# Kernel optimization log

Hardware: AMD Instinct MI355X
Metric: run time of the kernel (lower is better)

Reference implementation:

```python
import jax, jax.numpy as jnp
import numpy as np
import math

B, S, D, H = 4, 1024, 1024, 16
HD = D // H  # 64
DFF = 4 * D
LN_EPS = 1e-5

def setup_inputs() -> dict:
    key = jax.random.key(0)
    ks = jax.random.split(key, 24)
    sd = lambda fi, fo: 1.0 / math.sqrt(fi)
    def lin(k, fi, fo):
        k1, k2 = jax.random.split(k)
        w = jax.random.uniform(k1, (fi, fo), jnp.float32, -sd(fi, fo), sd(fi, fo))
        b = jax.random.uniform(k2, (fo,), jnp.float32, -sd(fi, fo), sd(fi, fo))
        return w, b
    x = jax.random.normal(ks[0], (B, S, D), jnp.float32)
    Wk, bk = lin(ks[1], D, D)
    Wq, bq = lin(ks[2], D, D)
    Wv, bv = lin(ks[3], D, D)
    # per-head projections stacked over heads: [H, D, HD]
    def head_lin(k):
        kk = jax.random.split(k, H)
        ws, bs = zip(*[lin(kk[h], D, HD) for h in range(H)])
        return jnp.stack(ws), jnp.stack(bs)
    Whq, bhq = head_lin(ks[4])
    Whk, bhk = head_lin(ks[5])
    Whv, bhv = head_lin(ks[6])
    Wo, bo = lin(ks[7], D, D)
    W1, b1 = lin(ks[8], D, DFF)
    W2, b2 = lin(ks[9], DFF, D)
    gamma = jnp.ones((D,), jnp.float32)
    beta = jnp.zeros((D,), jnp.float32)
    return dict(x=x, Wk=Wk, bk=bk, Wq=Wq, bq=bq, Wv=Wv, bv=bv,
                Whq=Whq, bhq=bhq, Whk=Whk, bhk=bhk, Whv=Whv, bhv=bhv,
                Wo=Wo, bo=bo, W1=W1, b1=b1, W2=W2, b2=b2,
                gamma=gamma, beta=beta)

def _layer_norm(x, gamma, beta):
    mu = jnp.mean(x, axis=-1, keepdims=True)
    var = jnp.mean(jnp.square(x - mu), axis=-1, keepdims=True)
    return (x - mu) * jax.lax.rsqrt(var + LN_EPS) * gamma + beta

def reference(x, Wk, bk, Wq, bq, Wv, bv, Whq, bhq, Whk, bhk, Whv, bhv,
              Wo, bo, W1, b1, W2, b2, gamma, beta):
    # outer projections; NOTE: forward passes (k, q, v) into MHA, so the
    # MHA 'Q' stream is k_proj(x), 'K' stream is q_proj(x), 'V' is v_proj(x)
    ko = x @ Wk + bk
    qo = x @ Wq + bq
    vo = x @ Wv + bv
    # per-head projections (batched over heads): [B,H,S,HD]
    q = jnp.einsum('bsd,hde->bhse', ko, Whq) + bhq[None, :, None, :]
    k = jnp.einsum('bsd,hde->bhse', qo, Whk) + bhk[None, :, None, :]
    v = jnp.einsum('bsd,hde->bhse', vo, Whv) + bhv[None, :, None, :]
    # NOTE: original scales by sqrt(d_model), not sqrt(head_dim)
    scores = jnp.einsum('bhse,bhte->bhst', q, k) / math.sqrt(D)
    w = jax.nn.softmax(scores, axis=-1)
    o = jnp.einsum('bhst,bhte->bhse', w, v)         # [B,H,S,HD]
    o = o.transpose(0, 2, 1, 3).reshape(B, S, D)    # concat heads
    attn = o @ Wo + bo
    # dropout is identity in eval; shared LayerNorm after both residuals
    r1 = _layer_norm(x + attn, gamma, beta)
    ff = jax.nn.gelu(r1 @ W1 + b1, approximate=False) @ W2 + b2
    out = _layer_norm(r1 + ff, gamma, beta)
    return out
```

## Files before the change

kernel.cpp:

```cpp
#include <hip/hip_runtime.h>
#include <cstdint>
#include <cstddef>

#define D_MODEL 1024
#define SEQ 1024
#define BATCH 4
#define NHEAD 16
#define HDIM 64
#define ROWS (BATCH*SEQ)

typedef unsigned short u16;
typedef __attribute__((ext_vector_type(4))) unsigned short u16x4;
typedef __attribute__((ext_vector_type(8))) unsigned short u16x8;
typedef __attribute__((ext_vector_type(8))) __bf16 bf16x8v;
typedef __attribute__((ext_vector_type(4))) float f32x4;

__device__ inline u16 f2bf(float f){
  union{float f; unsigned u;} c; c.f = f;
  unsigned r = c.u + 0x7FFFu + ((c.u>>16)&1u);
  return (u16)(r>>16);
}
__device__ inline float bf2f(u16 s){
  union{unsigned u; float f;} c; c.u = ((unsigned)s)<<16; return c.f;
}
__device__ inline float gelu_f(float x){ return 0.5f*x*(1.f+erff(x*0.7071067811865475f)); }

__device__ __forceinline__ void gload_lds16(const void* g, void* l){
  __builtin_amdgcn_global_load_lds(
    (const __attribute__((address_space(1))) unsigned int*)g,
    (__attribute__((address_space(3))) unsigned int*)l, 16, 0, 0);
}

__global__ __launch_bounds__(256) void convert_bf(const float* __restrict__ in, u16* __restrict__ out){
  size_t idx = (size_t)blockIdx.x*256 + threadIdx.x;
  f32x4 v = *(const f32x4*)(in + idx*4);
  u16x4 o = { f2bf(v.x), f2bf(v.y), f2bf(v.z), f2bf(v.w) };
  *(u16x4*)(out + idx*4) = o;
}

__global__ __launch_bounds__(256) void transpose_conv(const float* __restrict__ W, u16* __restrict__ WT, int K, int N){
  __shared__ float tile[32][33];
  int n0 = blockIdx.x*32, k0 = blockIdx.y*32;
  int tx = threadIdx.x & 31, ty = threadIdx.x >> 5;
  #pragma unroll
  for (int i=0;i<4;i++){
    int r = ty + i*8;
    tile[r][tx] = W[(size_t)(k0+r)*N + n0 + tx];
  }
  __syncthreads();
  #pragma unroll
  for (int i=0;i<4;i++){
    int r = ty + i*8;
    WT[(size_t)(n0+r)*K + k0 + tx] = f2bf(tile[tx][r]);
  }
}

__global__ __launch_bounds__(256) void head_transpose(const float* __restrict__ Wh, u16* __restrict__ WT){
  __shared__ float tile[32][33];
  int d0 = blockIdx.x*32, e0 = blockIdx.y*32, h = blockIdx.z;
  int tx = threadIdx.x & 31, ty = threadIdx.x >> 5;
  #pragma unroll
  for (int i=0;i<4;i++){
    int r = ty + i*8;
    tile[r][tx] = Wh[(size_t)h*D_MODEL*HDIM + (size_t)(d0+r)*HDIM + e0 + tx];
  }
  __syncthreads();
  #pragma unroll
  for (int i=0;i<4;i++){
    int r = ty + i*8;
    WT[(size_t)(h*HDIM + e0 + r)*D_MODEL + d0 + tx] = f2bf(tile[tx][r]);
  }
}

__global__ __launch_bounds__(256) void bias_cat(const float* a, const float* b, const float* c, float* o){
  int i = blockIdx.x*256 + threadIdx.x;
  float v = (i < 1024) ? a[i] : (i < 2048) ? b[i-1024] : c[i-2048];
  o[i] = v;
}

__device__ __forceinline__ void phase16(const u16* Ah, const u16* Bh,
  f32x4 acc[8][4], int mq, int nq, int wr, int wc, int fr, int kg)
{
  bf16x8v af[2][4], bfv[2][2];
  #pragma unroll
  for (int ks=0;ks<2;ks++){
    #pragma unroll
    for (int mf=0;mf<4;mf++){
      int r = wr*64 + mf*16 + fr;
      af[ks][mf] = *(const bf16x8v*)&Ah[r*64 + (((kg+4*ks)^(r&7)))*8];
    }
    #pragma unroll
    for (int nf=0;nf<2;nf++){
      int r = wc*32 + nf*16 + fr;
      bfv[ks][nf] = *(const bf16x8v*)&Bh[r*64 + (((kg+4*ks)^(r&7)))*8];
    }
  }
  __builtin_amdgcn_s_setprio(1);
  #pragma unroll
  for (int ks=0;ks<2;ks++)
    #pragma unroll
    for (int mf=0;mf<4;mf++)
      #pragma unroll
      for (int nf=0;nf<2;nf++)
        acc[mq*4+mf][nq*2+nf] =
          __builtin_amdgcn_mfma_f32_16x16x32_bf16(af[ks][mf], bfv[ks][nf], acc[mq*4+mf][nq*2+nf], 0,0,0);
  __builtin_amdgcn_s_setprio(0);
}

__global__ __launch_bounds__(512,2) void gemm256_8p(
  const u16* __restrict__ A, const u16* __restrict__ BT, const float* __restrict__ bias,
  u16* __restrict__ outB, int N, int K, int mode, int act)
{
  __shared__ __align__(16) u16 As[2][2][128*64];
  __shared__ __align__(16) u16 Bs[2][2][128*64];
  int t = threadIdx.x, lane = t&63, wid = t>>6;
  int wr = wid>>2, wc = wid&3;
  int fr = lane&15, kg = lane>>4;
  int gx = gridDim.x;
  int bid = blockIdx.y*gx + blockIdx.x;
  int nwg = gx*gridDim.y;
  int cpx = nwg>>3;
  int sw = (bid&7)*cpx + (bid>>3);
  int tc = sw % gx, tr = sw / gx;

  const u16* Abase = A  + (size_t)tr*256*K;
  const u16* Bbase = BT + (size_t)tc*256*K;
  int srow = lane>>3, sch8 = lane&7;

  f32x4 acc[8][4];
  #pragma unroll
  for (int m=0;m<8;m++)
    #pragma unroll
    for (int n=0;n<4;n++) acc[m][n] = (f32x4)0.f;

  #define STAGE_A8(buf,h,kt) { _Pragma("unroll") for (int li=0;li<2;li++){ \
    int sr = (wid*2+li)*8 + srow; \
    int gr = ((sr>>6)<<7) + (h)*64 + (sr&63); \
    int sc = sch8 ^ (sr&7); \
    gload_lds16(Abase + (size_t)gr*K + (size_t)(kt)*64 + sc*8, &As[buf][h][(wid*2+li)*512]); } }
  #define STAGE_B8(buf,h,kt) { _Pragma("unroll") for (int li=0;li<2;li++){ \
    int sr = (wid*2+li)*8 + srow; \
    int gc = ((sr>>5)<<6) + (h)*32 + (sr&31); \
    int sc = sch8 ^ (sr&7); \
    gload_lds16(Bbase + (size_t)gc*K + (size_t)(kt)*64 + sc*8, &Bs[buf][h][(wid*2+li)*512]); } }
  #define BAR asm volatile("s_barrier" ::: "memory")

  int NT = K >> 6;
  STAGE_A8(0,0,0); STAGE_B8(0,0,0); STAGE_B8(0,1,0); STAGE_A8(0,1,0);
  asm volatile("s_waitcnt vmcnt(4)" ::: "memory");

  for (int kt=0; kt<NT; ++kt){
    int buf = kt&1, nb = buf^1;
    int pre = (kt+1 < NT);
    if (pre) STAGE_A8(nb,0,kt+1);
    BAR;
    phase16(&As[buf][0][0], &Bs[buf][0][0], acc, 0,0, wr,wc,fr,kg);
    BAR;
    if (pre){ STAGE_B8(nb,0,kt+1); asm volatile("s_waitcnt vmcnt(6)" ::: "memory"); }
    else    { asm volatile("s_waitcnt vmcnt(2)" ::: "memory"); }
    BAR;
    phase16(&As[buf][0][0], &Bs[buf][1][0], acc, 0,1, wr,wc,fr,kg);
    BAR;
    if (pre){ STAGE_B8(nb,1,kt+1); asm volatile("s_waitcnt vmcnt(6)" ::: "memory"); }
    else    { asm volatile("s_waitcnt vmcnt(0)" ::: "memory"); }
    BAR;
    phase16(&As[buf][1][0], &Bs[buf][0][0], acc, 1,0, wr,wc,fr,kg);
    BAR;
    if (pre){ STAGE_A8(nb,1,kt+1); asm volatile("s_waitcnt vmcnt(4)" ::: "memory"); }
    BAR;
    phase16(&As[buf][1][0], &Bs[buf][1][0], acc, 1,1, wr,wc,fr,kg);
    BAR;
  }

  int crow0 = tr*256 + wr*128;
  int ccol0 = tc*256 + wc*64;
  #pragma unroll
  for (int n=0;n<4;n++){
    int col = ccol0 + n*16 + fr;
    float bv = bias[mode==0 ? col : (col & (N-1))];
    #pragma unroll
    for (int m=0;m<8;m++){
      int rbase = crow0 + m*16 + kg*4;
      #pragma unroll
      for (int i=0;i<4;i++){
        float v = acc[m][n][i] + bv;
        if (act) v = gelu_f(v);
        int row = rbase + i;
        if (mode == 0)
          outB[(size_t)(col>>10)*((size_t)ROWS*1024) + (size_t)row*1024 + (col&1023)] = f2bf(v);
        else
          outB[(size_t)row*N + col] = f2bf(v);
      }
    }
  }
}

__device__ __forceinline__ void stage128(u16 (*As)[4096], u16 (*Bs)[4096], int b,
  const u16* Ab, const u16* Bb, int Kstride, int kt, int wid, int rr, int sch)
{
  #pragma unroll
  for (int c=0;c<2;c++){
    int reg = c*4 + wid;
    int row = reg*16 + rr;
    gload_lds16(Ab + (size_t)row*Kstride + kt*32 + sch*8, &As[b][reg*512]);
  }
  #pragma unroll
  for (int c=0;c<2;c++){
    int reg = c*4 + wid;
    int row = reg*16 + rr;
    gload_lds16(Bb + (size_t)row*Kstride + kt*32 + sch*8, &Bs[b][reg*512]);
  }
}

__device__ __forceinline__ void gemm128_core(u16 (*As)[4096], u16 (*Bs)[4096],
  const u16* __restrict__ A, const u16* __restrict__ BT, const float* __restrict__ bias,
  float* __restrict__ outF, u16* __restrict__ outB,
  int N, int Kstride, int kofs, int Ksub, int mode, int act, int addbias)
{
  int t = threadIdx.x, lane = t&63, wid = t>>6;
  int wr = wid>>1, wc = wid&1;
  int fr = lane&15, kg = lane>>4;
  int gx = gridDim.x;
  int bid = blockIdx.y*gx + blockIdx.x;
  int nwg = gx*gridDim.y;
  int cpx = nwg >> 3;
  int sw = (bid&7)*cpx + (bid>>3);
  int tc = sw % gx, tr = sw / gx;

  const u16* Ab = A  + (size_t)tr*128*Kstride + kofs;
  const u16* Bb = BT + (size_t)tc*128*Kstride + kofs;
  int rr = lane>>2, cc = lane&3;
  int sch = cc ^ ((rr>>1)&3);

  f32x4 acc[4][4];
  #pragma unroll
  for (int m=0;m<4;m++)
    #pragma unroll
    for (int n=0;n<4;n++) acc[m][n] = (f32x4)0.f;

  int NT = Ksub >> 5;

  stage128(As, Bs, 0, Ab, Bb, Kstride, 0, wid, rr, sch);
  stage128(As, Bs, 1, Ab, Bb, Kstride, 1, wid, rr, sch);
  int buf = 0;
  for (int kt=0; kt<NT; ++kt){
    if (kt+2 < NT){
      int nb = buf+2; if (nb>=3) nb-=3;
      stage128(As, Bs, nb, Ab, Bb, Kstride, kt+2, wid, rr, sch);
      asm volatile("s_waitcnt vmcnt(8)" ::: "memory");
    } else if (kt+1 < NT){
      asm volatile("s_waitcnt vmcnt(4)" ::: "memory");
    } else {
      asm volatile("s_waitcnt vmcnt(0)" ::: "memory");
    }
    asm volatile("s_barrier" ::: "memory");
    bf16x8v af[4], bfv[4];
    #pragma unroll
    for (int m=0;m<4;m++){
      int r = wr*64 + m*16 + fr;
      af[m] = *(const bf16x8v*)&As[buf][r*32 + (kg ^ ((r>>1)&3))*8];
    }
    #pragma unroll
    for (int n=0;n<4;n++){
      int r = wc*64 + n*16 + fr;
      bfv[n] = *(const bf16x8v*)&Bs[buf][r*32 + (kg ^ ((r>>1)&3))*8];
    }
    #pragma unroll
    for (int m=0;m<4;m++)
      #pragma unroll
      for (int n=0;n<4;n++)
        acc[m][n] = __builtin_amdgcn_mfma_f32_16x16x32_bf16(af[m], bfv[n], acc[m][n], 0,0,0);
    if (kt+1 < NT)
      asm volatile("s_barrier" ::: "memory");
    buf += 1; if (buf >= 3) buf = 0;
  }

  int crow0 = tr*128 + wr*64;
  int ccol0 = tc*128 + wc*64;
  #pragma unroll
  for (int n=0;n<4;n++){
    int col = ccol0 + n*16 + fr;
    float bv = addbias ? bias[col] : 0.f;
    #pragma unroll
    for (int m=0;m<4;m++){
      int rbase = crow0 + m*16 + kg*4;
      #pragma unroll
      for (int i=0;i<4;i++){
        float v = acc[m][n][i] + bv;
        if (act) v = gelu_f(v);
        int row = rbase + i;
        if (mode == 0){
          outB[(size_t)(col>>10)*((size_t)ROWS*1024) + (size_t)row*1024 + (col&1023)] = f2bf(v);
        } else if (mode == 1){
          outB[(size_t)row*N + col] = f2bf(v);
        } else if (mode == 2){
          int b = row >> 10, s = row & 1023;
          int h = col >> 6, e = col & 63;
          outB[(((size_t)((b*NHEAD + h)*HDIM + e))<<10) + s] = f2bf(v);
        } else {
          outF[(size_t)row*1024 + col] = v;
        }
      }
    }
  }
}

__global__ __launch_bounds__(256) void g_gemm_sk(
  const u16* A, const u16* BT, const float* bias, float* outBase, int K)
{
  __shared__ __align__(16) u16 As[3][4096];
  __shared__ __align__(16) u16 Bs[3][4096];
  int z = blockIdx.z;
  int Ksub = K >> 1;
  gemm128_core(As, Bs, A, BT, bias, outBase + (size_t)z*ROWS*1024, nullptr,
               1024, K, z*Ksub, Ksub, 3, 0, z==0);
}

struct B3 { const u16* A[3]; const u16* BT[3]; const float* bias[3]; u16* Cb[3]; int mode[3]; };
__global__ __launch_bounds__(256) void g_gemm_b3(B3 p){
  __shared__ __align__(16) u16 As[3][4096];
  __shared__ __align__(16) u16 Bs[3][4096];
  int z = blockIdx.z;
  gemm128_core(As, Bs, p.A[z], p.BT[z], p.bias[z], nullptr, p.Cb[z],
               1024, 1024, 0, 1024, p.mode[z], 0, 1);
}

__global__ __launch_bounds__(256) void attn_mfma(const u16* __restrict__ Q, const u16* __restrict__ Km,
                                                 const u16* __restrict__ Vt, u16* __restrict__ O)
{
  __shared__ __align__(16) u16 Ks[64*64];
  __shared__ __align__(16) u16 Vs[64*64];
  __shared__ __align__(16) u16 Ps[4][16*64];
  int t = threadIdx.x, lane = t & 63, wid = t >> 6;
  int fr = lane & 15, kg = lane >> 4;
  int qt = blockIdx.x, h = blockIdx.y, b = blockIdx.z;
  const size_t qkbase = ((size_t)b*SEQ)*D_MODEL + (size_t)h*HDIM;
  const size_t vtb = ((size_t)(b*NHEAD + h))*HDIM*SEQ;

  int qrow = qt*64 + wid*16 + fr;
  bf16x8v aq[2];
  aq[0] = *(const bf16x8v*)(Q + qkbase + (size_t)qrow*D_MODEL + kg*8);
  aq[1] = *(const bf16x8v*)(Q + qkbase + (size_t)qrow*D_MODEL + 32 + kg*8);

  f32x4 Oacc[4];
  #pragma unroll
  for (int n=0;n<4;n++) Oacc[n] = (f32x4)0.f;
  float m_run[4], l_run[4];
  #pragma unroll
  for (int i=0;i<4;i++){ m_run[i] = -3e38f; l_run[i] = 0.f; }

  int srow = lane >> 3;
  int sch  = (lane & 7) ^ srow;
  int x7 = fr & 7;

  for (int kt = 0; kt < SEQ/64; ++kt){
    #pragma unroll
    for (int c=0;c<2;c++){
      int r0 = (wid*2 + c)*8;
      int rowk = r0 + srow;
      gload_lds16(Km + qkbase + (size_t)(kt*64 + rowk)*D_MODEL + sch*8, &Ks[r0*64]);
      gload_lds16(Vt + vtb + (size_t)rowk*SEQ + kt*64 + sch*8, &Vs[r0*64]);
    }
    __syncthreads();

    f32x4 z4 = (f32x4)0.f;
    f32x4 s4[4];
    #pragma unroll
    for (int n=0;n<4;n++){
      int r = n*16 + fr;
      bf16x8v k0v = *(const bf16x8v*)&Ks[r*64 + ((kg  ) ^ x7)*8];
      bf16x8v k1v = *(const bf16x8v*)&Ks[r*64 + ((4+kg) ^ x7)*8];
      s4[n] = __builtin_amdgcn_mfma_f32_16x16x32_bf16(aq[0], k0v, z4, 0,0,0);
      s4[n] = __builtin_amdgcn_mfma_f32_16x16x32_bf16(aq[1], k1v, s4[n], 0,0,0);
      s4[n] *= 0.03125f;
    }

    float mI[4], sc[4], ls[4], p[4][4];
    #pragma unroll
    for (int i=0;i<4;i++)
      mI[i] = fmaxf(fmaxf(s4[0][i], s4[1][i]), fmaxf(s4[2][i], s4[3][i]));
    #pragma unroll
    for (int off=1; off<16; off<<=1){
      #pragma unroll
      for (int i=0;i<4;i++) mI[i] = fmaxf(mI[i], __shfl_xor(mI[i], off));
    }
    #pragma unroll
    for (int i=0;i<4;i++){
      float m_new = fmaxf(m_run[i], mI[i]);
      sc[i] = __expf(m_run[i] - m_new);
      m_run[i] = m_new;
      ls[i] = 0.f;
    }
    #pragma unroll
    for (int n=0;n<4;n++)
      #pragma unroll
      for (int i=0;i<4;i++){
        float pv = __expf(s4[n][i] - m_run[i]);
        p[n][i] = pv;
        ls[i] += pv;
      }
    #pragma unroll
    for (int off=1; off<16; off<<=1){
      #pragma unroll
      for (int i=0;i<4;i++) ls[i] += __shfl_xor(ls[i], off);
    }
    #pragma unroll
    for (int i=0;i<4;i++) l_run[i] = l_run[i]*sc[i] + ls[i];
    #pragma unroll
    for (int n=0;n<4;n++)
      #pragma unroll
      for (int i=0;i<4;i++) Oacc[n][i] *= sc[i];

    u16* Pw = &Ps[wid][0];
    #pragma unroll
    for (int n=0;n<4;n++){
      int chunk = n*2 + (fr>>3);
      #pragma unroll
      for (int i=0;i<4;i++){
        int row = kg*4 + i;
        Pw[row*64 + (chunk ^ (row&7))*8 + (fr&7)] = f2bf(p[n][i]);
      }
    }
    asm volatile("s_waitcnt lgkmcnt(0)" ::: "memory");

    bf16x8v ap0 = *(const bf16x8v*)&Pw[fr*64 + ((kg  ) ^ x7)*8];
    bf16x8v ap1 = *(const bf16x8v*)&Pw[fr*64 + ((4+kg) ^ x7)*8];
    #pragma unroll
    for (int n2=0;n2<4;n2++){
      int r = n2*16 + fr;
      bf16x8v v0 = *(const bf16x8v*)&Vs[r*64 + ((kg  ) ^ x7)*8];
      bf16x8v v1 = *(const bf16x8v*)&Vs[r*64 + ((4+kg) ^ x7)*8];
      Oacc[n2] = __builtin_amdgcn_mfma_f32_16x16x32_bf16(ap0, v0, Oacc[n2], 0,0,0);
      Oacc[n2] = __builtin_amdgcn_mfma_f32_16x16x32_bf16(ap1, v1, Oacc[n2], 0,0,0);
    }
    __syncthreads();
  }

  float inv[4];
  #pragma unroll
  for (int i=0;i<4;i++) inv[i] = 1.f / l_run[i];
  #pragma unroll
  for (int n2=0;n2<4;n2++){
    #pragma unroll
    for (int i=0;i<4;i++){
      int row = qt*64 + wid*16 + kg*4 + i;
      O[qkbase + (size_t)row*D_MODEL + n2*16 + fr] = f2bf(Oacc[n2][i]*inv[i]);
    }
  }
}

__global__ __launch_bounds__(256) void ln_sum3(const float* __restrict__ A, const float* __restrict__ B,
   const float* __restrict__ C, const float* __restrict__ gamma, const float* __restrict__ beta,
   float* __restrict__ Of, u16* __restrict__ Ob)
{
  int row = blockIdx.x, t = threadIdx.x;
  size_t base = (size_t)row*D_MODEL + t*4;
  f32x4 v = *(const f32x4*)(A + base);
  v += *(const f32x4*)(B + base);
  v += *(const f32x4*)(C + base);
  float s = v.x+v.y+v.z+v.w;
  float q = v.x*v.x+v.y*v.y+v.z*v.z+v.w*v.w;
  #pragma unroll
  for (int off=1; off<64; off<<=1){ s += __shfl_xor(s,off); q += __shfl_xor(q,off); }
  __shared__ float red[8];
  int wid = t>>6;
  if ((t&63)==0){ red[wid] = s; red[wid+4] = q; }
  __syncthreads();
  s = red[0]+red[1]+red[2]+red[3];
  q = red[4]+red[5]+red[6]+red[7];
  float mu = s*(1.f/1024.f);
  float var = q*(1.f/1024.f) - mu*mu;
  float rs = rsqrtf(var + 1e-5f);
  f32x4 g4 = *(const f32x4*)(gamma + t*4);
  f32x4 b4 = *(const f32x4*)(beta + t*4);
  f32x4 o;
  o.x = (v.x-mu)*rs*g4.x + b4.x;
  o.y = (v.y-mu)*rs*g4.y + b4.y;
  o.z = (v.z-mu)*rs*g4.z + b4.z;
  o.w = (v.w-mu)*rs*g4.w + b4.w;
  if (Of) *(f32x4*)(Of + base) = o;
  if (Ob){
    u16x4 ob = { f2bf(o.x), f2bf(o.y), f2bf(o.z), f2bf(o.w) };
    *(u16x4*)(Ob + base) = ob;
  }
}

extern "C" void kernel_launch(void* const* d_in, const int* in_sizes, int n_in,
                              void* d_out, int out_size, void* d_ws, size_t ws_size,
                              hipStream_t stream)
{
  const float* x    = (const float*)d_in[0];
  const float* Wk   = (const float*)d_in[1];
  const float* bk   = (const float*)d_in[2];
  const float* Wq   = (const float*)d_in[3];
  const float* bq   = (const float*)d_in[4];
  const float* Wv   = (const float*)d_in[5];
  const float* bv   = (const float*)d_in[6];
  const float* Whq  = (const float*)d_in[7];
  const float* bhq  = (const float*)d_in[8];
  const float* Whk  = (const float*)d_in[9];
  const float* bhk  = (const float*)d_in[10];
  const float* Whv  = (const float*)d_in[11];
  const float* bhv  = (const float*)d_in[12];
  const float* Wo   = (const float*)d_in[13];
  const float* bo   = (const float*)d_in[14];
  const float* W1   = (const float*)d_in[15];
  const float* b1   = (const float*)d_in[16];
  const float* W2   = (const float*)d_in[17];
  const float* b2   = (const float*)d_in[18];
  const float* gamma= (const float*)d_in[19];
  const float* beta = (const float*)d_in[20];

  char* ws = (char*)d_ws;
  const size_t MB_ = 1024*1024;
  u16* WkT  = (u16*)(ws + 0*MB_);
  u16* WqT  = (u16*)(ws + 2*MB_);
  u16* WvT  = (u16*)(ws + 4*MB_);
  u16* WhqT = (u16*)(ws + 6*MB_);
  u16* WhkT = (u16*)(ws + 8*MB_);
  u16* WhvT = (u16*)(ws + 10*MB_);
  u16* WoT  = (u16*)(ws + 12*MB_);
  u16* W1T  = (u16*)(ws + 14*MB_);
  u16* W2T  = (u16*)(ws + 22*MB_);
  u16* xb   = (u16*)(ws + 30*MB_);
  u16* kob  = (u16*)(ws + 38*MB_);
  u16* qob  = (u16*)(ws + 46*MB_);
  u16* vob  = (u16*)(ws + 54*MB_);
  u16* qb   = (u16*)(ws + 62*MB_);
  u16* kb   = (u16*)(ws + 70*MB_);
  u16* vt   = (u16*)(ws + 78*MB_);
  u16* Ob   = (u16*)(ws + 86*MB_);
  u16* ff1b = (u16*)(ws + 38*MB_);
  float* r1f = (float*)(ws + 70*MB_);
  u16*  r1b  = (u16*)(ws + 86*MB_);
  float* P0  = (float*)(ws + 94*MB_);
  float* P1  = (float*)(ws + 110*MB_);
  float* bcat = (float*)(ws + 126*MB_);

  dim3 tb(256);

  convert_bf<<<dim3(ROWS*D_MODEL/4/256), tb, 0, stream>>>(x, xb);
  transpose_conv<<<dim3(32,32),  tb, 0, stream>>>(Wk, WkT, 1024, 1024);
  transpose_conv<<<dim3(32,32),  tb, 0, stream>>>(Wq, WqT, 1024, 1024);
  transpose_conv<<<dim3(32,32),  tb, 0, stream>>>(Wv, WvT, 1024, 1024);
  transpose_conv<<<dim3(32,32),  tb, 0, stream>>>(Wo, WoT, 1024, 1024);
  transpose_conv<<<dim3(128,32), tb, 0, stream>>>(W1, W1T, 1024, 4096);
  transpose_conv<<<dim3(32,128), tb, 0, stream>>>(W2, W2T, 4096, 1024);
  head_transpose<<<dim3(32,2,16), tb, 0, stream>>>(Whq, WhqT);
  head_transpose<<<dim3(32,2,16), tb, 0, stream>>>(Whk, WhkT);
  head_transpose<<<dim3(32,2,16), tb, 0, stream>>>(Whv, WhvT);
  bias_cat<<<dim3(12), tb, 0, stream>>>(bk, bq, bv, bcat);

  gemm256_8p<<<dim3(12,16), dim3(512), 0, stream>>>(xb, WkT, bcat, kob, 3072, 1024, 0, 0);

  B3 p2;
  p2.A[0]=kob; p2.A[1]=qob; p2.A[2]=vob;
  p2.BT[0]=WhqT; p2.BT[1]=WhkT; p2.BT[2]=WhvT;
  p2.bias[0]=bhq; p2.bias[1]=bhk; p2.bias[2]=bhv;
  p2.Cb[0]=qb; p2.Cb[1]=kb; p2.Cb[2]=vt;
  p2.mode[0]=1; p2.mode[1]=1; p2.mode[2]=2;
  g_gemm_b3<<<dim3(8,32,3), tb, 0, stream>>>(p2);

  attn_mfma<<<dim3(16,16,4), tb, 0, stream>>>(qb, kb, vt, Ob);

  g_gemm_sk<<<dim3(8,32,2), tb, 0, stream>>>(Ob, WoT, bo, P0, 1024);
  ln_sum3<<<dim3(4096), tb, 0, stream>>>(x, P0, P1, gamma, beta, r1f, r1b);
  gemm256_8p<<<dim3(16,16), dim3(512), 0, stream>>>(r1b, W1T, b1, ff1b, 4096, 1024, 1, 1);
  g_gemm_sk<<<dim3(8,32,2), tb, 0, stream>>>(ff1b, W2T, b2, P0, 4096);
  ln_sum3<<<dim3(4096), tb, 0, stream>>>(r1f, P0, P1, gamma, beta, (float*)d_out, nullptr);

  (void)in_sizes; (void)n_in; (void)out_size; (void)ws_size;
}
```

Measured before the change: 371.9 us.

## Reuse LDS fragments across GEMM phases and issue fragment loads before global staging

Removes the phase16 helper and inlines fragment loads into the main GEMM loop. A-fragments and B-fragments now stay in registers across consecutive quadrant phases, and the quadrant order is changed to (0,0),(0,1),(1,1),(1,0) so each phase reloads only one operand. The LDS reads are issued before the next tile's global-to-LDS staging and its vmcnt waits, so they overlap. This cuts LDS read traffic but changes the wait counts and barrier placement, which risks races or register pressure at 2 waves per SIMD.

```diff
diff --git a/kernel.cpp b/kernel.cpp
--- a/kernel.cpp
+++ b/kernel.cpp
@@ -76,35 +76,6 @@
   int i = blockIdx.x*256 + threadIdx.x;
   float v = (i < 1024) ? a[i] : (i < 2048) ? b[i-1024] : c[i-2048];
   o[i] = v;
-}
-
-__device__ __forceinline__ void phase16(const u16* Ah, const u16* Bh,
-  f32x4 acc[8][4], int mq, int nq, int wr, int wc, int fr, int kg)
-{
-  bf16x8v af[2][4], bfv[2][2];
-  #pragma unroll
-  for (int ks=0;ks<2;ks++){
-    #pragma unroll
-    for (int mf=0;mf<4;mf++){
-      int r = wr*64 + mf*16 + fr;
-      af[ks][mf] = *(const bf16x8v*)&Ah[r*64 + (((kg+4*ks)^(r&7)))*8];
-    }
-    #pragma unroll
-    for (int nf=0;nf<2;nf++){
-      int r = wc*32 + nf*16 + fr;
-      bfv[ks][nf] = *(const bf16x8v*)&Bh[r*64 + (((kg+4*ks)^(r&7)))*8];
-    }
-  }
-  __builtin_amdgcn_s_setprio(1);
-  #pragma unroll
-  for (int ks=0;ks<2;ks++)
-    #pragma unroll
-    for (int mf=0;mf<4;mf++)
-      #pragma unroll
-      for (int nf=0;nf<2;nf++)
-        acc[mq*4+mf][nq*2+nf] =
-          __builtin_amdgcn_mfma_f32_16x16x32_bf16(af[ks][mf], bfv[ks][nf], acc[mq*4+mf][nq*2+nf], 0,0,0);
-  __builtin_amdgcn_s_setprio(0);
 }
 
 __global__ __launch_bounds__(512,2) void gemm256_8p(
@@ -133,6 +104,8 @@
     #pragma unroll
     for (int n=0;n<4;n++) acc[m][n] = (f32x4)0.f;
 
+  bf16x8v af[2][4], bfv[2][2];
+
   #define STAGE_A8(buf,h,kt) { _Pragma("unroll") for (int li=0;li<2;li++){ \
     int sr = (wid*2+li)*8 + srow; \
     int gr = ((sr>>6)<<7) + (h)*64 + (sr&63); \
@@ -143,33 +116,41 @@
     int gc = ((sr>>5)<<6) + (h)*32 + (sr&31); \
     int sc = sch8 ^ (sr&7); \
     gload_lds16(Bbase + (size_t)gc*K + (size_t)(kt)*64 + sc*8, &Bs[buf][h][(wid*2+li)*512]); } }
+  #define LDA8(buf,h) { _Pragma("unroll") for (int ks=0;ks<2;ks++) _Pragma("unroll") for (int mf=0;mf<4;mf++){ \
+    int r = wr*64 + mf*16 + fr; \
+    af[ks][mf] = *(const bf16x8v*)&As[buf][h][r*64 + (((kg+4*ks)^(r&7)))*8]; } }
+  #define LDB8(buf,h) { _Pragma("unroll") for (int ks=0;ks<2;ks++) _Pragma("unroll") for (int nf=0;nf<2;nf++){ \
+    int r = wc*32 + nf*16 + fr; \
+    bfv[ks][nf] = *(const bf16x8v*)&Bs[buf][h][r*64 + (((kg+4*ks)^(r&7)))*8]; } }
+  #define MM8(mq,nq) { asm volatile("s_waitcnt lgkmcnt(0)" ::: "memory"); \
+    __builtin_amdgcn_s_setprio(1); \
+    _Pragma("unroll") for (int ks=0;ks<2;ks++) _Pragma("unroll") for (int mf=0;mf<4;mf++) _Pragma("unroll") for (int nf=0;nf<2;nf++) \
+      acc[(mq)*4+mf][(nq)*2+nf] = __builtin_amdgcn_mfma_f32_16x16x32_bf16(af[ks][mf], bfv[ks][nf], acc[(mq)*4+mf][(nq)*2+nf], 0,0,0); \
+    __builtin_amdgcn_s_setprio(0); }
   #define BAR asm volatile("s_barrier" ::: "memory")
 
   int NT = K >> 6;
   STAGE_A8(0,0,0); STAGE_B8(0,0,0); STAGE_B8(0,1,0); STAGE_A8(0,1,0);
   asm volatile("s_waitcnt vmcnt(4)" ::: "memory");
+  BAR;
 
   for (int kt=0; kt<NT; ++kt){
     int buf = kt&1, nb = buf^1;
     int pre = (kt+1 < NT);
-    if (pre) STAGE_A8(nb,0,kt+1);
-    BAR;
-    phase16(&As[buf][0][0], &Bs[buf][0][0], acc, 0,0, wr,wc,fr,kg);
-    BAR;
-    if (pre){ STAGE_B8(nb,0,kt+1); asm volatile("s_waitcnt vmcnt(6)" ::: "memory"); }
-    else    { asm volatile("s_waitcnt vmcnt(2)" ::: "memory"); }
-    BAR;
-    phase16(&As[buf][0][0], &Bs[buf][1][0], acc, 0,1, wr,wc,fr,kg);
-    BAR;
+    LDA8(buf,0); LDB8(buf,0);
+    if (pre){ STAGE_A8(nb,0,kt+1); asm volatile("s_waitcnt vmcnt(4)" ::: "memory"); }
+    else    {                      asm volatile("s_waitcnt vmcnt(2)" ::: "memory"); }
+    BAR; MM8(0,0); BAR;
+    LDB8(buf,1);
+    if (pre){ STAGE_B8(nb,0,kt+1); asm volatile("s_waitcnt vmcnt(4)" ::: "memory"); }
+    else    {                      asm volatile("s_waitcnt vmcnt(0)" ::: "memory"); }
+    BAR; MM8(0,1); BAR;
+    LDA8(buf,1);
     if (pre){ STAGE_B8(nb,1,kt+1); asm volatile("s_waitcnt vmcnt(6)" ::: "memory"); }
-    else    { asm volatile("s_waitcnt vmcnt(0)" ::: "memory"); }
-    BAR;
-    phase16(&As[buf][1][0], &Bs[buf][0][0], acc, 1,0, wr,wc,fr,kg);
-    BAR;
+    BAR; MM8(1,1); BAR;
+    LDB8(buf,0);
     if (pre){ STAGE_A8(nb,1,kt+1); asm volatile("s_waitcnt vmcnt(4)" ::: "memory"); }
-    BAR;
-    phase16(&As[buf][1][0], &Bs[buf][1][0], acc, 1,1, wr,wc,fr,kg);
-    BAR;
+    BAR; MM8(1,0); BAR;
   }
 
   int crow0 = tr*256 + wr*128;
```

After: 333.6 us. -10.3%, faster.
